# Performance work log

Hardware: AMD Instinct MI355X
Metric: run time of the kernel (lower is better)

Reference implementation:

```python
import jax, jax.numpy as jnp
import numpy as np

N = 50000    # nodes
E = 800000   # edges (avg degree 16)
IN = 256     # in_dim
HID = 256    # hidden_dim
OUT = 128    # out_dim


def setup_inputs() -> dict:
    key = jax.random.key(0)
    ks = jax.random.split(key, 9)
    features = jax.random.normal(ks[0], (N, IN), jnp.float32)
    src = jax.random.randint(ks[1], (E,), 0, N, jnp.int32)
    dst = jax.random.randint(ks[2], (E,), 0, N, jnp.int32)
    noise = jax.random.normal(ks[3], (N, OUT), jnp.float32)
    def glorot(k, shape, fan):
        return jax.random.normal(k, shape, jnp.float32) / np.float32(np.sqrt(fan))
    W1 = glorot(ks[4], (IN, HID), IN);  b1 = jnp.zeros((HID,), jnp.float32)
    W2 = glorot(ks[5], (HID, OUT), HID); b2 = jnp.zeros((OUT,), jnp.float32)
    W3 = glorot(ks[6], (HID, OUT), HID); b3 = jnp.zeros((OUT,), jnp.float32)
    fcW = glorot(ks[7], (HID, IN), IN)   # nn.Linear(in_dim, hidden_dim).weight: [HID, IN]
    return dict(features=features, noise=noise, W1=W1, b1=b1, W2=W2, b2=b2,
                W3=W3, b3=b3, fcW=fcW, src=src, dst=dst)


def _gcn(x, W, b, src, dst, out_norm, in_norm):
    """DGL GraphConv norm='both': D_out^{-1/2} A D_in^{-1/2} X W + b."""
    x = x * out_norm[:, None]          # scale src features by out-deg^{-1/2}
    x = x @ W                          # dense transform (order commutes with SpMM)
    agg = jax.ops.segment_sum(x[src], dst, num_segments=N)  # sparse aggregate
    return agg * in_norm[:, None] + b


def reference(features, noise, W1, b1, W2, b2, W3, b3, fcW, src, dst):
    ones = jnp.ones((E,), jnp.float32)
    out_deg = jax.ops.segment_sum(ones, src, num_segments=N)
    in_deg = jax.ops.segment_sum(ones, dst, num_segments=N)
    out_norm = jnp.maximum(out_deg, 1.0) ** -0.5
    in_norm = jnp.maximum(in_deg, 1.0) ** -0.5

    h = jax.nn.relu(_gcn(features, W1, b1, src, dst, out_norm, in_norm))
    mean = jax.nn.relu(_gcn(h, W2, b2, src, dst, out_norm, in_norm))
    log_std = _gcn(h, W3, b3, src, dst, out_norm, in_norm)  # identity activation
    z = mean + noise * jnp.exp(log_std)
    seq_fts = features @ fcW.T
    return z, h, seq_fts
```

## Files before the change

### kernel.cpp

```cpp
#include <hip/hip_runtime.h>
#include <hip/hip_bf16.h>
#include <stdint.h>
#include <math.h>

#define IN_DIM 256
#define HID_DIM 256
#define OUT_DIM 128

typedef __attribute__((ext_vector_type(8))) short short8;
typedef __attribute__((ext_vector_type(4))) float floatx4;

__device__ __forceinline__ float bf2f(ushort u) {
  union { uint32_t i; float f; } v; v.i = ((uint32_t)u) << 16; return v.f;
}
__device__ __forceinline__ ushort f2bf(float f) {
  union { float f; uint32_t u; } v; v.f = f;
  uint32_t u = v.u;
  uint32_t r = u + 0x7fffu + ((u >> 16) & 1u);
  return (ushort)(r >> 16);
}

__global__ void deg_prep_kernel(const int* __restrict__ src, const int* __restrict__ dst,
                                int* __restrict__ out_deg, int* __restrict__ in_deg,
                                int E, int eblocks,
                                const float* __restrict__ W1, const float* __restrict__ W2,
                                const float* __restrict__ W3, const float* __restrict__ b2,
                                const float* __restrict__ b3,
                                ushort* __restrict__ W1T, ushort* __restrict__ WcT,
                                float* __restrict__ bcat) {
  int b = blockIdx.x, t = threadIdx.x;
  if (b < eblocks) {
    int e = (b * 256 + t) * 2;
    if (e + 1 < E) {
      int2 s = *(const int2*)(src + e);
      int2 d = *(const int2*)(dst + e);
      atomicAdd(&out_deg[s.x], 1);
      atomicAdd(&out_deg[s.y], 1);
      atomicAdd(&in_deg[d.x], 1);
      atomicAdd(&in_deg[d.y], 1);
    } else if (e < E) {
      atomicAdd(&out_deg[src[e]], 1);
      atomicAdd(&in_deg[dst[e]], 1);
    }
  } else {
    int k = b - eblocks;
    int nn = t;
    W1T[nn * 256 + k] = f2bf(W1[k * 256 + nn]);
    WcT[nn * 256 + k] = f2bf((nn < 128) ? W2[k * 128 + nn] : W3[k * 128 + (nn - 128)]);
    if (k == 0) bcat[nn] = (nn < 128) ? b2[nn] : b3[nn - 128];
  }
}

__global__ __launch_bounds__(256, 2) void mega_kernel(
    const float* __restrict__ feat, const float* __restrict__ fcW,
    const ushort* __restrict__ W1T,
    float* __restrict__ s_out, ushort* __restrict__ xw1_bf,
    const int* __restrict__ in_deg, int* __restrict__ row_ptr, int n, int M, int gb) {
  __shared__ alignas(16) ushort A_lds[128 * 72];
  __shared__ alignas(16) ushort B_lds[256 * 72];
  int b = blockIdx.x;
  int t = threadIdx.x;

  if (b == 0) {
    int* lds = (int*)A_lds;
    int CH = (n + 255) >> 8; CH = (CH + 3) & ~3;
    int base = t * CH;
    int s = 0;
    if (base + CH <= n) {
      const int4* p = (const int4*)(in_deg + base);
      int c4 = CH >> 2;
#pragma unroll 8
      for (int j = 0; j < c4; ++j) { int4 q = p[j]; s += q.x + q.y + q.z + q.w; }
    } else {
      for (int i = base; i < n; ++i) s += in_deg[i];
    }
    lds[t] = s;
    __syncthreads();
    for (int off = 1; off < 256; off <<= 1) {
      int add = (t >= off) ? lds[t - off] : 0;
      __syncthreads();
      lds[t] += add;
      __syncthreads();
    }
    int run = lds[t] - s;
    if (t == 0) row_ptr[0] = 0;
    if (base + CH <= n) {
      const int4* p = (const int4*)(in_deg + base);
      int c4 = CH >> 2;
#pragma unroll 4
      for (int j = 0; j < c4; ++j) {
        int4 q = p[j];
        int i = base + j * 4;
        run += q.x; row_ptr[i + 1] = run;
        run += q.y; row_ptr[i + 2] = run;
        run += q.z; row_ptr[i + 3] = run;
        run += q.w; row_ptr[i + 4] = run;
      }
    } else {
      for (int i = base; i < n; ++i) { run += in_deg[i]; row_ptr[i + 1] = run; }
    }
    return;
  }

  int bb = b - 1;
  bool isSeq = bb < gb;
  int m0 = (isSeq ? bb : bb - gb) * 128;
  int wave = t >> 6, lane = t & 63;
  int wm = wave * 32;
  int l15 = lane & 15, quad = lane >> 4;

  floatx4 acc[2][16];
#pragma unroll
  for (int i = 0; i < 2; ++i)
#pragma unroll
    for (int j = 0; j < 16; ++j) acc[i][j] = (floatx4)(0.f);

  for (int kc = 0; kc < 256; kc += 64) {
#pragma unroll
    for (int r = 0; r < 8; ++r) {
      int idx = t + r * 256;
      int row = idx >> 4;
      int c = (idx & 15) << 2;
      int grow = m0 + row; if (grow > M - 1) grow = M - 1;
      float4 v = *(const float4*)(feat + (size_t)grow * 256 + kc + c);
      ushort4 o;
      o.x = f2bf(v.x); o.y = f2bf(v.y); o.z = f2bf(v.z); o.w = f2bf(v.w);
      *(ushort4*)&A_lds[row * 72 + c] = o;
    }
    if (isSeq) {
#pragma unroll
      for (int r = 0; r < 16; ++r) {
        int idx = t + r * 256;
        int row = idx >> 4;
        int c = (idx & 15) << 2;
        float4 v = *(const float4*)(fcW + (size_t)row * 256 + kc + c);
        ushort4 o;
        o.x = f2bf(v.x); o.y = f2bf(v.y); o.z = f2bf(v.z); o.w = f2bf(v.w);
        *(ushort4*)&B_lds[row * 72 + c] = o;
      }
    } else {
#pragma unroll
      for (int r = 0; r < 8; ++r) {
        int idx = t + r * 256;
        int row = idx >> 3;
        int c = (idx & 7) << 3;
        *(uint4*)&B_lds[row * 72 + c] = *(const uint4*)(W1T + (size_t)row * 256 + kc + c);
      }
    }
    __syncthreads();
#pragma unroll
    for (int ko = 0; ko < 2; ++ko) {
      short8 a[2];
#pragma unroll
      for (int i = 0; i < 2; ++i)
        a[i] = *(const short8*)&A_lds[(wm + i * 16 + l15) * 72 + ko * 32 + quad * 8];
#pragma unroll
      for (int j = 0; j < 16; ++j) {
        short8 bv = *(const short8*)&B_lds[(j * 16 + l15) * 72 + ko * 32 + quad * 8];
#pragma unroll
        for (int i = 0; i < 2; ++i)
          acc[i][j] = __builtin_amdgcn_mfma_f32_16x16x32_bf16(a[i], bv, acc[i][j], 0, 0, 0);
      }
    }
    __syncthreads();
  }

  if (isSeq) {
#pragma unroll
    for (int i = 0; i < 2; ++i)
#pragma unroll
      for (int j = 0; j < 16; ++j) {
        int col = j * 16 + l15;
#pragma unroll
        for (int r = 0; r < 4; ++r) {
          int row = m0 + wm + i * 16 + quad * 4 + r;
          if (row < M) s_out[(size_t)row * 256 + col] = acc[i][j][r];
        }
      }
  } else {
#pragma unroll
    for (int i = 0; i < 2; ++i)
#pragma unroll
      for (int j = 0; j < 16; ++j) {
        int col = j * 16 + l15;
#pragma unroll
        for (int r = 0; r < 4; ++r) {
          int row = m0 + wm + i * 16 + quad * 4 + r;
          if (row < M) xw1_bf[(size_t)row * 256 + col] = f2bf(acc[i][j][r]);
        }
      }
  }
}

__global__ void fill_kernel(const int* __restrict__ src, const int* __restrict__ dst,
                            const int* __restrict__ row_ptr, int* __restrict__ fill_cnt,
                            const int* __restrict__ out_deg,
                            int2* __restrict__ edge_sw, int E) {
  int e = (blockIdx.x * 256 + threadIdx.x) * 2;
  if (e + 1 < E) {
    int2 s = *(const int2*)(src + e);
    int2 d = *(const int2*)(dst + e);
    int pos0 = row_ptr[d.x] + atomicAdd(&fill_cnt[d.x], 1);
    int od0 = out_deg[s.x]; if (od0 < 1) od0 = 1;
    int2 r0; r0.x = s.x; r0.y = __float_as_int(rsqrtf((float)od0));
    edge_sw[pos0] = r0;
    int pos1 = row_ptr[d.y] + atomicAdd(&fill_cnt[d.y], 1);
    int od1 = out_deg[s.y]; if (od1 < 1) od1 = 1;
    int2 r1; r1.x = s.y; r1.y = __float_as_int(rsqrtf((float)od1));
    edge_sw[pos1] = r1;
  } else if (e < E) {
    int d = dst[e]; int s = src[e];
    int pos = row_ptr[d] + atomicAdd(&fill_cnt[d], 1);
    int od = out_deg[s]; if (od < 1) od = 1;
    int2 r; r.x = s; r.y = __float_as_int(rsqrtf((float)od));
    edge_sw[pos] = r;
  }
}

__global__ __launch_bounds__(256) void agg_kernel(
    const ushort* __restrict__ x, const int* __restrict__ row_ptr,
    const int2* __restrict__ edge_sw,
    const float* __restrict__ bias, const float* __restrict__ noise,
    float* __restrict__ out32, ushort* __restrict__ outbf, int N, int mode) {
  int wave = threadIdx.x >> 6, lane = threadIdx.x & 63;
  int n = blockIdx.x * 4 + wave;
  if (n >= N) return;
  int half = lane >> 5;
  int hl = lane & 31;
  int start = row_ptr[n], end = row_ptr[n + 1];
  int dg = end - start; if (dg < 1) dg = 1;
  float inn = rsqrtf((float)dg);

  float acc[8];
#pragma unroll
  for (int k = 0; k < 8; ++k) acc[k] = 0.f;

  for (int base = start; base < end; base += 16) {
    int cs[8]; float cw[8];
    if (base + 16 <= end) {
#pragma unroll
      for (int k = 0; k < 8; ++k) {
        int2 e = edge_sw[base + half + 2 * k];
        cs[k] = e.x; cw[k] = __int_as_float(e.y);
      }
    } else {
#pragma unroll
      for (int k = 0; k < 8; ++k) {
        int i = base + half + 2 * k;
        cs[k] = 0; cw[k] = 0.f;
        if (i < end) { int2 e = edge_sw[i]; cs[k] = e.x; cw[k] = __int_as_float(e.y); }
      }
    }
    uint4 v[8];
#pragma unroll
    for (int k = 0; k < 8; ++k)
      v[k] = *(const uint4*)&x[(size_t)cs[k] * 256 + hl * 8];
#pragma unroll
    for (int k = 0; k < 8; ++k) {
      const uint32_t* p = (const uint32_t*)&v[k];
      float wk = cw[k];
#pragma unroll
      for (int q = 0; q < 4; ++q) {
        acc[2 * q]     += bf2f((ushort)(p[q] & 0xffffu)) * wk;
        acc[2 * q + 1] += bf2f((ushort)(p[q] >> 16)) * wk;
      }
    }
  }

#pragma unroll
  for (int k = 0; k < 8; ++k) acc[k] += __shfl_xor(acc[k], 32, 64);

  if (mode == 0) {
    if (half == 0) {
      int c0 = hl * 8;
      float4 ba = *(const float4*)(bias + c0);
      float4 bb = *(const float4*)(bias + c0 + 4);
      float h[8];
      h[0] = fmaxf(acc[0] * inn + ba.x, 0.f);
      h[1] = fmaxf(acc[1] * inn + ba.y, 0.f);
      h[2] = fmaxf(acc[2] * inn + ba.z, 0.f);
      h[3] = fmaxf(acc[3] * inn + ba.w, 0.f);
      h[4] = fmaxf(acc[4] * inn + bb.x, 0.f);
      h[5] = fmaxf(acc[5] * inn + bb.y, 0.f);
      h[6] = fmaxf(acc[6] * inn + bb.z, 0.f);
      h[7] = fmaxf(acc[7] * inn + bb.w, 0.f);
      float4 o0 = make_float4(h[0], h[1], h[2], h[3]);
      float4 o1 = make_float4(h[4], h[5], h[6], h[7]);
      *(float4*)&out32[(size_t)n * 256 + c0] = o0;
      *(float4*)&out32[(size_t)n * 256 + c0 + 4] = o1;
      uint4 ob; uint32_t* po = (uint32_t*)&ob;
#pragma unroll
      for (int q = 0; q < 4; ++q)
        po[q] = ((uint32_t)f2bf(h[2 * q + 1]) << 16) | (uint32_t)f2bf(h[2 * q]);
      *(uint4*)&outbf[(size_t)n * 256 + c0] = ob;
    }
  } else {
    float pacc[8];
#pragma unroll
    for (int k = 0; k < 8; ++k) pacc[k] = __shfl(acc[k], (lane & 15) + 16, 64);
    if (lane < 16) {
      int c0 = lane * 8;
      float4 b2a = *(const float4*)(bias + c0);
      float4 b2b = *(const float4*)(bias + c0 + 4);
      float4 b3a = *(const float4*)(bias + 128 + c0);
      float4 b3b = *(const float4*)(bias + 128 + c0 + 4);
      float4 nza = *(const float4*)(noise + (size_t)n * 128 + c0);
      float4 nzb = *(const float4*)(noise + (size_t)n * 128 + c0 + 4);
      float z[8];
      z[0] = fmaxf(acc[0] * inn + b2a.x, 0.f) + nza.x * expf(pacc[0] * inn + b3a.x);
      z[1] = fmaxf(acc[1] * inn + b2a.y, 0.f) + nza.y * expf(pacc[1] * inn + b3a.y);
      z[2] = fmaxf(acc[2] * inn + b2a.z, 0.f) + nza.z * expf(pacc[2] * inn + b3a.z);
      z[3] = fmaxf(acc[3] * inn + b2a.w, 0.f) + nza.w * expf(pacc[3] * inn + b3a.w);
      z[4] = fmaxf(acc[4] * inn + b2b.x, 0.f) + nzb.x * expf(pacc[4] * inn + b3b.x);
      z[5] = fmaxf(acc[5] * inn + b2b.y, 0.f) + nzb.y * expf(pacc[5] * inn + b3b.y);
      z[6] = fmaxf(acc[6] * inn + b2b.z, 0.f) + nzb.z * expf(pacc[6] * inn + b3b.z);
      z[7] = fmaxf(acc[7] * inn + b2b.w, 0.f) + nzb.w * expf(pacc[7] * inn + b3b.w);
      *(float4*)&out32[(size_t)n * 128 + c0] = make_float4(z[0], z[1], z[2], z[3]);
      *(float4*)&out32[(size_t)n * 128 + c0 + 4] = make_float4(z[4], z[5], z[6], z[7]);
    }
  }
}

__global__ __launch_bounds__(256, 2) void gemm_bf_kernel(
    const ushort* __restrict__ A, const ushort* __restrict__ BT,
    ushort* __restrict__ Cbf, int M) {
  __shared__ alignas(16) ushort A_lds[128 * 72];
  __shared__ alignas(16) ushort B_lds[256 * 72];
  int t = threadIdx.x;
  int m0 = blockIdx.x * 128;
  int wave = t >> 6, lane = t & 63;
  int wm = wave * 32;
  int l15 = lane & 15, quad = lane >> 4;

  floatx4 acc[2][16];
#pragma unroll
  for (int i = 0; i < 2; ++i)
#pragma unroll
    for (int j = 0; j < 16; ++j) acc[i][j] = (floatx4)(0.f);

  for (int kc = 0; kc < 256; kc += 64) {
#pragma unroll
    for (int r = 0; r < 4; ++r) {
      int idx = t + r * 256;
      int row = idx >> 3;
      int c = (idx & 7) << 3;
      int grow = m0 + row; if (grow > M - 1) grow = M - 1;
      *(uint4*)&A_lds[row * 72 + c] = *(const uint4*)(A + (size_t)grow * 256 + kc + c);
    }
#pragma unroll
    for (int r = 0; r < 8; ++r) {
      int idx = t + r * 256;
      int row = idx >> 3;
      int c = (idx & 7) << 3;
      *(uint4*)&B_lds[row * 72 + c] = *(const uint4*)(BT + (size_t)row * 256 + kc + c);
    }
    __syncthreads();
#pragma unroll
    for (int ko = 0; ko < 2; ++ko) {
      short8 a[2];
#pragma unroll
      for (int i = 0; i < 2; ++i)
        a[i] = *(const short8*)&A_lds[(wm + i * 16 + l15) * 72 + ko * 32 + quad * 8];
#pragma unroll
      for (int j = 0; j < 16; ++j) {
        short8 bv = *(const short8*)&B_lds[(j * 16 + l15) * 72 + ko * 32 + quad * 8];
#pragma unroll
        for (int i = 0; i < 2; ++i)
          acc[i][j] = __builtin_amdgcn_mfma_f32_16x16x32_bf16(a[i], bv, acc[i][j], 0, 0, 0);
      }
    }
    __syncthreads();
  }

#pragma unroll
  for (int i = 0; i < 2; ++i)
#pragma unroll
    for (int j = 0; j < 16; ++j) {
      int col = j * 16 + l15;
#pragma unroll
      for (int r = 0; r < 4; ++r) {
        int row = m0 + wm + i * 16 + quad * 4 + r;
        if (row < M) Cbf[(size_t)row * 256 + col] = f2bf(acc[i][j][r]);
      }
    }
}

extern "C" void kernel_launch(void* const* d_in, const int* in_sizes, int n_in,
                              void* d_out, int out_size, void* d_ws, size_t ws_size,
                              hipStream_t stream) {
  const float* features = (const float*)d_in[0];
  const float* noise    = (const float*)d_in[1];
  const float* W1 = (const float*)d_in[2];
  const float* b1 = (const float*)d_in[3];
  const float* W2 = (const float*)d_in[4];
  const float* b2 = (const float*)d_in[5];
  const float* W3 = (const float*)d_in[6];
  const float* b3 = (const float*)d_in[7];
  const float* fcW = (const float*)d_in[8];
  const int* src = (const int*)d_in[9];
  const int* dst = (const int*)d_in[10];
  const int N = in_sizes[0] / IN_DIM;
  const int E = in_sizes[9];

  float* out = (float*)d_out;
  float* z_out = out;
  float* h_out = out + (size_t)N * OUT_DIM;
  float* s_out = h_out + (size_t)N * HID_DIM;

  char* w = (char*)d_ws;
  auto carve = [&](size_t bytes) {
    char* p = w;
    w += (bytes + 255) & ~(size_t)255;
    return p;
  };
  ushort* xw1_bf = (ushort*)carve((size_t)N * 256 * 2);
  ushort* h_bf   = (ushort*)carve((size_t)N * 256 * 2);
  ushort* hwc_bf = (ushort*)carve((size_t)N * 256 * 2);
  ushort* W1T  = (ushort*)carve(256 * 256 * 2);
  ushort* WcT  = (ushort*)carve(256 * 256 * 2);
  float*  bcat = (float*)carve(256 * 4);
  int* degs    = (int*)carve((size_t)3 * N * 4);
  int* out_deg = degs;
  int* in_deg  = degs + N;
  int* fill_cnt = degs + 2 * N;
  int* row_ptr  = (int*)carve((size_t)(N + 1) * 4);
  int2* edge_sw = (int2*)carve((size_t)E * 8);

  hipMemsetAsync(degs, 0, (size_t)3 * N * 4, stream);
  int eblocks = ((E + 1) / 2 + 255) / 256;
  int gb = (N + 127) / 128;

  deg_prep_kernel<<<eblocks + 256, 256, 0, stream>>>(src, dst, out_deg, in_deg, E, eblocks,
                                                     W1, W2, W3, b2, b3, W1T, WcT, bcat);
  mega_kernel<<<2 * gb + 1, 256, 0, stream>>>(features, fcW, W1T, s_out, xw1_bf,
                                              in_deg, row_ptr, N, N, gb);
  fill_kernel<<<eblocks, 256, 0, stream>>>(src, dst, row_ptr, fill_cnt, out_deg,
                                           edge_sw, E);
  agg_kernel<<<(N + 3) / 4, 256, 0, stream>>>(xw1_bf, row_ptr, edge_sw, b1,
                                              (const float*)nullptr, h_out, h_bf, N, 0);
  gemm_bf_kernel<<<gb, 256, 0, stream>>>(h_bf, WcT, hwc_bf, N);
  agg_kernel<<<(N + 3) / 4, 256, 0, stream>>>(hwc_bf, row_ptr, edge_sw, bcat,
                                              noise, z_out, (ushort*)nullptr, N, 1);
}
```

Before: 508.7 us.

## Pre-convert fcW to bf16 and use XOR-swizzled unpadded LDS tiles in GEMMs

Converts fcW to bf16 once in the prep kernel, so the seq GEMM blocks load B as bf16 like the W1 path instead of reconverting fp32 weights in every block. The padded 72-stride LDS layout becomes a 64-stride layout with XOR column swizzling, which shrinks shared memory per block while avoiding bank conflicts. Launch bounds go from 2 to 3 blocks per CU to use the freed LDS for occupancy, at the risk of register pressure or spills with the 32-accumulator tiles.

```diff
diff --git a/kernel.cpp b/kernel.cpp
--- a/kernel.cpp
+++ b/kernel.cpp
@@ -25,9 +25,9 @@
                                 int E, int eblocks,
                                 const float* __restrict__ W1, const float* __restrict__ W2,
                                 const float* __restrict__ W3, const float* __restrict__ b2,
-                                const float* __restrict__ b3,
+                                const float* __restrict__ b3, const float* __restrict__ fcW,
                                 ushort* __restrict__ W1T, ushort* __restrict__ WcT,
-                                float* __restrict__ bcat) {
+                                float* __restrict__ bcat, ushort* __restrict__ fcWb) {
   int b = blockIdx.x, t = threadIdx.x;
   if (b < eblocks) {
     int e = (b * 256 + t) * 2;
@@ -42,22 +42,25 @@
       atomicAdd(&out_deg[src[e]], 1);
       atomicAdd(&in_deg[dst[e]], 1);
     }
-  } else {
+  } else if (b < eblocks + 256) {
     int k = b - eblocks;
     int nn = t;
     W1T[nn * 256 + k] = f2bf(W1[k * 256 + nn]);
     WcT[nn * 256 + k] = f2bf((nn < 128) ? W2[k * 128 + nn] : W3[k * 128 + (nn - 128)]);
     if (k == 0) bcat[nn] = (nn < 128) ? b2[nn] : b3[nn - 128];
-  }
-}
-
-__global__ __launch_bounds__(256, 2) void mega_kernel(
-    const float* __restrict__ feat, const float* __restrict__ fcW,
+  } else {
+    int k = b - eblocks - 256;
+    fcWb[k * 256 + t] = f2bf(fcW[k * 256 + t]);
+  }
+}
+
+__global__ __launch_bounds__(256, 3) void mega_kernel(
+    const float* __restrict__ feat, const ushort* __restrict__ fcWb,
     const ushort* __restrict__ W1T,
     float* __restrict__ s_out, ushort* __restrict__ xw1_bf,
     const int* __restrict__ in_deg, int* __restrict__ row_ptr, int n, int M, int gb) {
-  __shared__ alignas(16) ushort A_lds[128 * 72];
-  __shared__ alignas(16) ushort B_lds[256 * 72];
+  __shared__ alignas(16) ushort A_lds[128 * 64];
+  __shared__ alignas(16) ushort B_lds[256 * 64];
   int b = blockIdx.x;
   int t = threadIdx.x;
 
@@ -105,6 +108,7 @@
   int bb = b - 1;
   bool isSeq = bb < gb;
   int m0 = (isSeq ? bb : bb - gb) * 128;
+  const ushort* Bsrc = isSeq ? fcWb : W1T;
   int wave = t >> 6, lane = t & 63;
   int wm = wave * 32;
   int l15 = lane & 15, quad = lane >> 4;
@@ -125,38 +129,32 @@
       float4 v = *(const float4*)(feat + (size_t)grow * 256 + kc + c);
       ushort4 o;
       o.x = f2bf(v.x); o.y = f2bf(v.y); o.z = f2bf(v.z); o.w = f2bf(v.w);
-      *(ushort4*)&A_lds[row * 72 + c] = o;
-    }
-    if (isSeq) {
-#pragma unroll
-      for (int r = 0; r < 16; ++r) {
-        int idx = t + r * 256;
-        int row = idx >> 4;
-        int c = (idx & 15) << 2;
-        float4 v = *(const float4*)(fcW + (size_t)row * 256 + kc + c);
-        ushort4 o;
-        o.x = f2bf(v.x); o.y = f2bf(v.y); o.z = f2bf(v.z); o.w = f2bf(v.w);
-        *(ushort4*)&B_lds[row * 72 + c] = o;
-      }
-    } else {
-#pragma unroll
-      for (int r = 0; r < 8; ++r) {
-        int idx = t + r * 256;
-        int row = idx >> 3;
-        int c = (idx & 7) << 3;
-        *(uint4*)&B_lds[row * 72 + c] = *(const uint4*)(W1T + (size_t)row * 256 + kc + c);
-      }
+      int sc = c ^ ((row & 7) << 3);
+      *(ushort4*)&A_lds[row * 64 + sc] = o;
+    }
+#pragma unroll
+    for (int r = 0; r < 8; ++r) {
+      int idx = t + r * 256;
+      int row = idx >> 3;
+      int c = (idx & 7) << 3;
+      int sc = c ^ ((row & 7) << 3);
+      *(uint4*)&B_lds[row * 64 + sc] = *(const uint4*)(Bsrc + (size_t)row * 256 + kc + c);
     }
     __syncthreads();
 #pragma unroll
     for (int ko = 0; ko < 2; ++ko) {
       short8 a[2];
 #pragma unroll
-      for (int i = 0; i < 2; ++i)
-        a[i] = *(const short8*)&A_lds[(wm + i * 16 + l15) * 72 + ko * 32 + quad * 8];
+      for (int i = 0; i < 2; ++i) {
+        int row = wm + i * 16 + l15;
+        int sc = (ko * 32 + quad * 8) ^ ((l15 & 7) << 3);
+        a[i] = *(const short8*)&A_lds[row * 64 + sc];
+      }
 #pragma unroll
       for (int j = 0; j < 16; ++j) {
-        short8 bv = *(const short8*)&B_lds[(j * 16 + l15) * 72 + ko * 32 + quad * 8];
+        int brow = j * 16 + l15;
+        int sc = (ko * 32 + quad * 8) ^ ((l15 & 7) << 3);
+        short8 bv = *(const short8*)&B_lds[brow * 64 + sc];
 #pragma unroll
         for (int i = 0; i < 2; ++i)
           acc[i][j] = __builtin_amdgcn_mfma_f32_16x16x32_bf16(a[i], bv, acc[i][j], 0, 0, 0);
@@ -284,10 +282,8 @@
       h[5] = fmaxf(acc[5] * inn + bb.y, 0.f);
       h[6] = fmaxf(acc[6] * inn + bb.z, 0.f);
       h[7] = fmaxf(acc[7] * inn + bb.w, 0.f);
-      float4 o0 = make_float4(h[0], h[1], h[2], h[3]);
-      float4 o1 = make_float4(h[4], h[5], h[6], h[7]);
-      *(float4*)&out32[(size_t)n * 256 + c0] = o0;
-      *(float4*)&out32[(size_t)n * 256 + c0 + 4] = o1;
+      *(float4*)&out32[(size_t)n * 256 + c0] = make_float4(h[0], h[1], h[2], h[3]);
+      *(float4*)&out32[(size_t)n * 256 + c0 + 4] = make_float4(h[4], h[5], h[6], h[7]);
       uint4 ob; uint32_t* po = (uint32_t*)&ob;
 #pragma unroll
       for (int q = 0; q < 4; ++q)
@@ -321,11 +317,11 @@
   }
 }
 
-__global__ __launch_bounds__(256, 2) void gemm_bf_kernel(
+__global__ __launch_bounds__(256, 3) void gemm_bf_kernel(
     const ushort* __restrict__ A, const ushort* __restrict__ BT,
     ushort* __restrict__ Cbf, int M) {
-  __shared__ alignas(16) ushort A_lds[128 * 72];
-  __shared__ alignas(16) ushort B_lds[256 * 72];
+  __shared__ alignas(16) ushort A_lds[128 * 64];
+  __shared__ alignas(16) ushort B_lds[256 * 64];
   int t = threadIdx.x;
   int m0 = blockIdx.x * 128;
   int wave = t >> 6, lane = t & 63;
@@ -345,25 +341,32 @@
       int row = idx >> 3;
       int c = (idx & 7) << 3;
       int grow = m0 + row; if (grow > M - 1) grow = M - 1;
-      *(uint4*)&A_lds[row * 72 + c] = *(const uint4*)(A + (size_t)grow * 256 + kc + c);
+      int sc = c ^ ((row & 7) << 3);
+      *(uint4*)&A_lds[row * 64 + sc] = *(const uint4*)(A + (size_t)grow * 256 + kc + c);
     }
 #pragma unroll
     for (int r = 0; r < 8; ++r) {
       int idx = t + r * 256;
       int row = idx >> 3;
       int c = (idx & 7) << 3;
-      *(uint4*)&B_lds[row * 72 + c] = *(const uint4*)(BT + (size_t)row * 256 + kc + c);
+      int sc = c ^ ((row & 7) << 3);
+      *(uint4*)&B_lds[row * 64 + sc] = *(const uint4*)(BT + (size_t)row * 256 + kc + c);
     }
     __syncthreads();
 #pragma unroll
     for (int ko = 0; ko < 2; ++ko) {
       short8 a[2];
 #pragma unroll
-      for (int i = 0; i < 2; ++i)
-        a[i] = *(const short8*)&A_lds[(wm + i * 16 + l15) * 72 + ko * 32 + quad * 8];
+      for (int i = 0; i < 2; ++i) {
+        int row = wm + i * 16 + l15;
+        int sc = (ko * 32 + quad * 8) ^ ((l15 & 7) << 3);
+        a[i] = *(const short8*)&A_lds[row * 64 + sc];
+      }
 #pragma unroll
       for (int j = 0; j < 16; ++j) {
-        short8 bv = *(const short8*)&B_lds[(j * 16 + l15) * 72 + ko * 32 + quad * 8];
+        int brow = j * 16 + l15;
+        int sc = (ko * 32 + quad * 8) ^ ((l15 & 7) << 3);
+        short8 bv = *(const short8*)&B_lds[brow * 64 + sc];
 #pragma unroll
         for (int i = 0; i < 2; ++i)
           acc[i][j] = __builtin_amdgcn_mfma_f32_16x16x32_bf16(a[i], bv, acc[i][j], 0, 0, 0);
@@ -418,6 +421,7 @@
   ushort* hwc_bf = (ushort*)carve((size_t)N * 256 * 2);
   ushort* W1T  = (ushort*)carve(256 * 256 * 2);
   ushort* WcT  = (ushort*)carve(256 * 256 * 2);
+  ushort* fcWb = (ushort*)carve(256 * 256 * 2);
   float*  bcat = (float*)carve(256 * 4);
   int* degs    = (int*)carve((size_t)3 * N * 4);
   int* out_deg = degs;
@@ -430,9 +434,10 @@
   int eblocks = ((E + 1) / 2 + 255) / 256;
   int gb = (N + 127) / 128;
 
-  deg_prep_kernel<<<eblocks + 256, 256, 0, stream>>>(src, dst, out_deg, in_deg, E, eblocks,
-                                                     W1, W2, W3, b2, b3, W1T, WcT, bcat);
-  mega_kernel<<<2 * gb + 1, 256, 0, stream>>>(features, fcW, W1T, s_out, xw1_bf,
+  deg_prep_kernel<<<eblocks + 512, 256, 0, stream>>>(src, dst, out_deg, in_deg, E, eblocks,
+                                                     W1, W2, W3, b2, b3, fcW,
+                                                     W1T, WcT, bcat, fcWb);
+  mega_kernel<<<2 * gb + 1, 256, 0, stream>>>(features, fcWb, W1T, s_out, xw1_bf,
                                               in_deg, row_ptr, N, N, gb);
   fill_kernel<<<eblocks, 256, 0, stream>>>(src, dst, row_ptr, fill_cnt, out_deg,
                                            edge_sw, E);
```

After: 584.7 us. 14.9% more time.
